# Performance work log

Hardware: AMD Instinct MI355X
Metric: run time of the kernel (lower is better)

Reference implementation:

```python
import jax, jax.numpy as jnp
import numpy as np
from jax import lax

# ---- config (matches DecodePredictions init kwargs) ----
MAX_PER_CLASS = 100
MAX_TOTAL = 100
IOU_THRESH = 0.5
SCORE_THRESH = 0.05
NUM_CLASSES = 80
K_CAND = 512  # per-class candidate pool kept before NMS (bounds the O(K^2) IoU work)
BOX_VARIANCE = np.array([0.1, 0.1, 0.2, 0.2], np.float32)


def generate_anchors(height, width):
    """RetinaNet anchors (keras.io AnchorBox): FPN levels 3-7, 3 ratios x 3 scales, [cx,cy,w,h] in pixels."""
    ratios = [0.5, 1.0, 2.0]
    scales = [2 ** 0.0, 2 ** (1.0 / 3.0), 2 ** (2.0 / 3.0)]
    all_anchors = []
    for level in range(3, 8):
        stride = 2 ** level
        area = float((2 ** (level + 2)) ** 2)  # 32^2 .. 512^2
        dims = []
        for r in ratios:
            ah = np.sqrt(area / r)
            aw = area / ah
            for s in scales:
                dims.append([s * aw, s * ah])
        dims = np.asarray(dims, np.float32)  # [9, 2] = (w, h)
        fh = int(np.ceil(height / stride))
        fw = int(np.ceil(width / stride))
        rx = (np.arange(fw, dtype=np.float32) + 0.5) * stride
        ry = (np.arange(fh, dtype=np.float32) + 0.5) * stride
        cx, cy = np.meshgrid(rx, ry)
        centers = np.stack([cx, cy], -1)[:, :, None, :].repeat(9, axis=2)  # [fh,fw,9,2]
        d = np.broadcast_to(dims, (fh, fw, 9, 2))
        all_anchors.append(np.concatenate([centers, d], -1).reshape(-1, 4).astype(np.float32))
    return jnp.asarray(np.concatenate(all_anchors, 0))  # [N, 4]


def _pairwise_iou(b):
    # Generic TF NMS IoU formula treating coords as [y1,x1,y2,x2] (module feeds cx,cy,w,h -- replicated faithfully).
    y1, x1, y2, x2 = b[:, 0], b[:, 1], b[:, 2], b[:, 3]
    area = jnp.maximum(y2 - y1, 0.0) * jnp.maximum(x2 - x1, 0.0)
    ih = jnp.maximum(jnp.minimum(y2[:, None], y2[None, :]) - jnp.maximum(y1[:, None], y1[None, :]), 0.0)
    iw = jnp.maximum(jnp.minimum(x2[:, None], x2[None, :]) - jnp.maximum(x1[:, None], x1[None, :]), 0.0)
    inter = ih * iw
    union = area[:, None] + area[None, :] - inter
    return jnp.where(union > 0.0, inter / union, 0.0)


def _nms_single_class(boxes, scores):  # boxes [N,4], scores [N]
    top_s, idx = lax.top_k(scores, K_CAND)          # sort-by-score candidate pool
    top_b = boxes[idx]                               # [K,4]
    keep0 = top_s > SCORE_THRESH                     # score_threshold filter
    iou = _pairwise_iou(top_b)                       # [K,K]
    rng = jnp.arange(K_CAND)

    def body(i, keep):
        sup = (iou[i] > IOU_THRESH) & (rng > i)      # boxes ranked below i suppressed by i
        return jnp.where(keep[i], keep & ~sup, keep)

    keep = lax.fori_loop(0, K_CAND, body, keep0)
    kept_s = jnp.where(keep, top_s, 0.0)
    sel_s, sel = lax.top_k(kept_s, MAX_PER_CLASS)    # max_output_size_per_class
    return top_b[sel], sel_s                         # [P,4], [P]


def _combine(cls_boxes, cls_scores):  # [C,P,4], [C,P] -> combined top MAX_TOTAL for one image
    C, P = cls_scores.shape
    flat_s = cls_scores.reshape(-1)
    flat_b = cls_boxes.reshape(-1, 4)
    flat_c = jnp.repeat(jnp.arange(C, dtype=jnp.float32), P)
    top_s, idx = lax.top_k(flat_s, MAX_TOTAL)
    valid = (top_s > 0.0)
    vf = valid.astype(flat_b.dtype)
    boxes = jnp.clip(flat_b[idx], 0.0, 1.0) * vf[:, None]  # clip_boxes=True, zero-pad invalid
    scores = top_s * vf
    classes = jnp.where(valid, flat_c[idx], 0.0)
    return boxes, scores, classes, valid.sum().astype(jnp.int32)


def _forward(inputs, predictions):
    H, W = inputs.shape[1], inputs.shape[2]
    anchors = generate_anchors(float(H), float(W))            # [N,4] cx,cy,w,h
    cls_scores = jax.nn.sigmoid(predictions[..., :-4])        # [B,N,C]
    box_pred = predictions[..., -4:] * jnp.asarray(BOX_VARIANCE)
    xy = box_pred[..., :2] * anchors[..., 2:] + anchors[..., :2]
    wh = jnp.exp(box_pred[..., 2:]) * anchors[..., 2:]
    boxes = jnp.concatenate([xy, wh], -1)                     # [B,N,4] decoded

    per_class = jax.vmap(jax.vmap(_nms_single_class, in_axes=(None, 1)), in_axes=(0, 0))
    cb, cs = per_class(boxes, cls_scores)                     # [B,C,P,4], [B,C,P]
    return jax.vmap(_combine)(cb, cs)                         # boxes, scores, classes, valid


def setup_inputs() -> dict:
    key = jax.random.key(0)
    k1, k2 = jax.random.split(key)
    inputs = jax.random.uniform(k1, (4, 640, 640, 3), jnp.float32)
    predictions = jax.random.normal(k2, (4, 76725, NUM_CLASSES + 4), jnp.float32)
    return {"inputs": inputs, "predictions": predictions}


def reference(inputs, predictions):
    return _forward(inputs, predictions)
```

## Files before the change

kernel.cpp:

```cpp
#include <hip/hip_runtime.h>
#include <cmath>

#define NA 76725
#define NCLS 80
#define NB 4
#define KC 512
#define MPC 100
#define MT 100
#define TT 64
#define LROW 85
#define NTILE 1199
#define NSLOTP 1199
#define NSLOTPAD 1216
#define PADN 76800
#define CAP 4096
#define SLOT 16
#define SPLIT 8
#define THRESH_LOGIT 2.0f

struct Dims { float d[5 * 9 * 2]; };


__device__ __forceinline__ unsigned keyof(float x) {
    unsigned u = __float_as_uint(x);
    return u ^ ((u & 0x80000000u) ? 0xFFFFFFFFu : 0x80000000u);
}
__device__ __forceinline__ float unkey(unsigned k) {
    unsigned u = (k & 0x80000000u) ? (k ^ 0x80000000u) : ~k;
    return __uint_as_float(u);
}
__device__ __forceinline__ float sigmoidf_dev(float x) {
    if (x >= 0.f) return 1.f / (1.f + expf(-x));
    float e = expf(x);
    return e / (1.f + e);
}
__device__ __forceinline__ unsigned long long compose(unsigned key, int a) {
    return ((unsigned long long)key << 32) | (unsigned long long)(0xFFFFFFFFu - (unsigned)a);
}

__device__ __forceinline__ float4 decode_box(float4 p, int a, const Dims& dims) {
    const int base[5] = {0, 57600, 72000, 75600, 76500};
    const int fw[5] = {80, 40, 20, 10, 5};
    const float strd[5] = {8.f, 16.f, 32.f, 64.f, 128.f};
    int l;
    if (a < 57600) l = 0;
    else if (a < 72000) l = 1;
    else if (a < 75600) l = 2;
    else if (a < 76500) l = 3;
    else l = 4;
    int i = a - base[l];
    int cell = i / 9, k = i - cell * 9;
    int x = cell % fw[l], y = cell / fw[l];
    float cx = ((float)x + 0.5f) * strd[l];
    float cy = ((float)y + 0.5f) * strd[l];
    float aw = dims.d[(l * 9 + k) * 2 + 0];
    float ah = dims.d[(l * 9 + k) * 2 + 1];
    float bx = __fmul_rn(p.x, 0.1f), by = __fmul_rn(p.y, 0.1f);
    float bw = __fmul_rn(p.z, 0.2f), bh = __fmul_rn(p.w, 0.2f);
    float4 o;
    o.x = __fadd_rn(__fmul_rn(bx, aw), cx);
    o.y = __fadd_rn(__fmul_rn(by, ah), cy);
    o.z = __fmul_rn(expf(bw), aw);
    o.w = __fmul_rn(expf(bh), ah);
    return o;
}


__global__ __launch_bounds__(256) void scan_kernel(const float* __restrict__ pred,
                                                   unsigned long long* __restrict__ candbuf,
                                                   int* __restrict__ counts2) {
    __shared__ float tile[TT * LROW];
    const int blk = blockIdx.x;
    const int b = blk / NTILE, tix = blk - b * NTILE;
    const int t0 = tix * TT;
    int nrow = NA - t0; if (nrow > TT) nrow = TT;

    const float4* src = reinterpret_cast<const float4*>(pred + ((size_t)b * NA + t0) * 84);
    const int nv = nrow * 21;
    for (int i = threadIdx.x; i < nv; i += 256) {
        float4 v = src[i];
        const int row = i / 21, fo = (i - row * 21) * 4;
        float* dst = &tile[row * LROW + fo];
        dst[0] = v.x; dst[1] = v.y; dst[2] = v.z; dst[3] = v.w;
    }
    __syncthreads();

    const int wv = threadIdx.x >> 6, lane = threadIdx.x & 63;
    const int c0 = wv * 20;
    const bool valid = lane < nrow;
    const int a = t0 + lane;
    const float* rowp = &tile[lane * LROW];

    int mycnt = 0;
    #pragma unroll
    for (int j = 0; j < 20; ++j) {
        const float x = valid ? rowp[c0 + j] : -1e30f;
        const bool hit = x > THRESH_LOGIT;
        const unsigned long long m = __ballot(hit);
        if (lane == j) mycnt = __popcll(m);
        if (hit) {
            const int rank = __popcll(m & ((1ull << lane) - 1ull));
            if (rank < SLOT) {
                const int col = b * NCLS + c0 + j;
                candbuf[((size_t)col * NSLOTP + tix) * SLOT + rank] = compose(keyof(x), a);
            }
        }
    }
    if (lane < 20)
        counts2[(size_t)(b * NCLS + c0 + lane) * NSLOTP + tix] = mycnt;
}


__device__ __forceinline__ void find_bin(int* hist, int bins, int remaining,
                                         int* sh3, int* wsum) {
    const int tid = threadIdx.x;
    const int lane = tid & 63, wv = tid >> 6;
    const int nit = (bins + 1023) >> 10;
    int lsum = 0;
    for (int q = 0; q < nit; ++q) {
        int rr = tid * nit + q;
        if (rr < bins) lsum += hist[bins - 1 - rr];
    }
    int acc = lsum;
    #pragma unroll
    for (int off = 1; off < 64; off <<= 1) {
        int x = __shfl_up(acc, off);
        if (lane >= off) acc += x;
    }
    if (lane == 63) wsum[wv] = acc;
    __syncthreads();
    int base = 0;
    for (int w = 0; w < wv; ++w) base += wsum[w];
    int run = base + acc - lsum;
    for (int q = 0; q < nit; ++q) {
        int rr = tid * nit + q;
        if (rr < bins) {
            int h = hist[bins - 1 - rr];
            if (run < remaining && remaining <= run + h) { sh3[0] = bins - 1 - rr; sh3[1] = run; sh3[2] = h; }
            run += h;
        }
    }
    __syncthreads();
}


__global__ __launch_bounds__(1024) void topk2_kernel(const float* __restrict__ pred,
                                                     const unsigned long long* __restrict__ candbuf,
                                                     const int* __restrict__ counts2,
                                                     int* __restrict__ top_idx,
                                                     float* __restrict__ top_score,
                                                     float4* __restrict__ sel_boxes, Dims dims) {
    const int col = blockIdx.x;
    const int b = col / NCLS, cc = col - b * NCLS;
    const int tid = threadIdx.x;
    const int lane = tid & 63, wv = tid >> 6;

    __shared__ unsigned long long cand[CAP];
    __shared__ int hist[256];
    __shared__ unsigned long long buf[KC];
    __shared__ int scnt[NSLOTPAD];
    __shared__ int spfx[NSLOTPAD];
    __shared__ int sh3[3];
    __shared__ int wsum[16];
    __shared__ int gcount, eqtaken, totsh, ovfsh;
    __shared__ int wcnt[16];
    int* hist4k = (int*)cand;

    for (int i = tid; i < NSLOTP; i += 1024)
        scnt[i] = counts2[(size_t)col * NSLOTP + i];
    if (tid < NSLOTPAD - NSLOTP) scnt[NSLOTP + tid] = 0;
    if (tid == 0) { totsh = 0; ovfsh = 0; }
    __syncthreads();

    const int e0 = 2 * tid, e1 = 2 * tid + 1;
    int c0s = 0, c1s = 0;
    if (e0 < NSLOTPAD) { c0s = scnt[e0]; c1s = scnt[e1]; }
    if (c0s > SLOT || c1s > SLOT) ovfsh = 1;
    const int pair = c0s + c1s;
    int acc = pair;
    #pragma unroll
    for (int off = 1; off < 64; off <<= 1) {
        int x = __shfl_up(acc, off);
        if (lane >= off) acc += x;
    }
    if (lane == 63) wsum[wv] = acc;
    __syncthreads();
    int base = 0;
    for (int w = 0; w < wv; ++w) base += wsum[w];
    if (e0 < NSLOTPAD) {
        const int excl = base + acc - pair;
        spfx[e0] = excl;
        spfx[e1] = excl + c0s;
    }
    if (tid == 1023) totsh = base + acc;
    __syncthreads();

    const int tot = totsh;
    const bool fastok = (!ovfsh) && tot >= KC && tot <= CAP;
    int nc = -1;

    if (fastok) {
        const unsigned long long* src = candbuf + (size_t)col * NSLOTP * SLOT;
        for (int i = tid; i < NSLOTP * SLOT; i += 1024) {
            const int e = i >> 4, q = i & (SLOT - 1);
            const unsigned long long v = src[i];
            if (q < scnt[e]) cand[spfx[e] + q] = v;
        }
        nc = tot;
        __syncthreads();
    } else {
        const float* colp = pred + (size_t)b * NA * 84 + cc;
        for (int i = tid; i < 4096; i += 1024) hist4k[i] = 0;
        __syncthreads();
        for (int a = tid; a < NA; a += 1024)
            atomicAdd(&hist4k[keyof(colp[(size_t)a * 84]) >> 20], 1);
        __syncthreads();
        find_bin(hist4k, 4096, KC, sh3, wsum);
        const int bsel = sh3[0], above = sh3[1], ceq1 = sh3[2];
        const int ncand = above + ceq1;

        if (ncand <= CAP) {
            const unsigned fk = ((unsigned)bsel) << 20;
            if (tid == 0) gcount = 0;
            __syncthreads();
            for (int a = tid; a < NA; a += 1024) {
                unsigned k = keyof(colp[(size_t)a * 84]);
                if (k >= fk) { int p = atomicAdd(&gcount, 1); cand[p] = compose(k, a); }
            }
            __syncthreads();
            nc = gcount;
        } else {
            unsigned prefix = ((unsigned)bsel) << 20;
            int remaining = KC - above;

            for (int i = tid; i < 4096; i += 1024) hist4k[i] = 0;
            __syncthreads();
            for (int a = tid; a < NA; a += 1024) {
                unsigned k = keyof(colp[(size_t)a * 84]);
                if ((k & 0xFFF00000u) == prefix) atomicAdd(&hist4k[(k >> 8) & 4095], 1);
            }
            __syncthreads();
            find_bin(hist4k, 4096, remaining, sh3, wsum);
            prefix |= ((unsigned)sh3[0]) << 8;
            remaining -= sh3[1];

            if (tid < 256) hist[tid] = 0;
            __syncthreads();
            for (int a = tid; a < NA; a += 1024) {
                unsigned k = keyof(colp[(size_t)a * 84]);
                if ((k & 0xFFFFFF00u) == prefix) atomicAdd(&hist[k & 255], 1);
            }
            __syncthreads();
            find_bin(hist, 256, remaining, sh3, wsum);
            prefix |= (unsigned)sh3[0];
            remaining -= sh3[1];

            const unsigned K = prefix;
            const int cgt = KC - remaining;
            const int need = remaining;
            if (tid == 0) { gcount = 0; eqtaken = 0; }
            __syncthreads();
            for (int bs = 0; bs < PADN; bs += 1024) {
                int a = bs + tid;
                unsigned key = (a < NA) ? keyof(colp[(size_t)a * 84]) : 0u;
                if (a < NA && key > K) {
                    int p = atomicAdd(&gcount, 1);
                    buf[p] = compose(key, a);
                }
                bool eq = (key == K) && (a < NA);
                unsigned long long m = __ballot(eq);
                if (lane == 0) wcnt[wv] = __popcll(m);
                __syncthreads();
                int off = eqtaken;
                for (int w = 0; w < wv; ++w) off += wcnt[w];
                int rank = off + __popcll(m & ((1ull << lane) - 1ull));
                if (eq && rank < need)
                    buf[cgt + rank] = compose(K, a);
                __syncthreads();
                if (tid == 0) {
                    int s = 0;
                    for (int w = 0; w < 16; ++w) s += wcnt[w];
                    eqtaken += s;
                }
                __syncthreads();
            }
            nc = -1;
        }
    }

    if (nc >= 0) {
        unsigned long long cpre = 0ull;
        int rem512 = KC;
        for (int pass = 0; pass < 8; ++pass) {
            const int shift = 56 - 8 * pass;
            const unsigned long long mdone = pass ? ((~0ull) << (shift + 8)) : 0ull;
            if (tid < 256) hist[tid] = 0;
            __syncthreads();
            for (int t = tid; t < nc; t += 1024) {
                unsigned long long k = cand[t];
                if ((k & mdone) == cpre) atomicAdd(&hist[(int)((k >> shift) & 255)], 1);
            }
            __syncthreads();
            find_bin(hist, 256, rem512, sh3, wsum);
            cpre |= ((unsigned long long)(unsigned)sh3[0]) << shift;
            rem512 -= sh3[1];
            __syncthreads();
        }
        if (tid == 0) gcount = 0;
        __syncthreads();
        for (int t = tid; t < nc; t += 1024) {
            unsigned long long k = cand[t];
            if (k >= cpre) { int p = atomicAdd(&gcount, 1); buf[p] = k; }
        }
        __syncthreads();
    }

    for (int k2 = 2; k2 <= KC; k2 <<= 1) {
        for (int j = k2 >> 1; j > 0; j >>= 1) {
            __syncthreads();
            if (tid < KC) {
                int i = tid, ixj = i ^ j;
                if (ixj > i) {
                    unsigned long long A = buf[i], B = buf[ixj];
                    bool up = (i & k2) == 0;
                    if (up ? (A < B) : (A > B)) { buf[i] = B; buf[ixj] = A; }
                }
            }
        }
    }
    __syncthreads();
    if (tid < KC) {
        unsigned long long v = buf[tid];
        unsigned key = (unsigned)(v >> 32);
        int a = (int)(0xFFFFFFFFu - (unsigned)(v & 0xFFFFFFFFu));
        top_idx[col * KC + tid] = a;
        top_score[col * KC + tid] = sigmoidf_dev(unkey(key));
        const float4 p4 = *reinterpret_cast<const float4*>(pred + ((size_t)b * NA + a) * 84 + 80);
        sel_boxes[(size_t)col * KC + tid] = decode_box(p4, a, dims);
    }
}


__global__ __launch_bounds__(512) void nms_build_kernel(const float4* __restrict__ sel_boxes,
                                                        unsigned long long* __restrict__ maskbuf) {
    const int blk = blockIdx.x;
    const int col = blk >> 3, part = blk & 7;
    const int tid = threadIdx.x, wave = tid >> 6, lane = tid & 63;
    __shared__ float y1[KC], x1[KC], y2[KC], x2[KC], ar[KC];

    for (int t = tid; t < KC; t += 512) {
        float4 bx = sel_boxes[(size_t)col * KC + t];
        y1[t] = bx.x; x1[t] = bx.y; y2[t] = bx.z; x2[t] = bx.w;
        ar[t] = __fmul_rn(fmaxf(__fsub_rn(bx.z, bx.x), 0.f),
                          fmaxf(__fsub_rn(bx.w, bx.y), 0.f));
    }
    __syncthreads();

    float jy1[8], jx1[8], jy2[8], jx2[8], jar[8];
    #pragma unroll
    for (int w = 0; w < 8; ++w) {
        int j = (w << 6) + lane;
        jy1[w] = y1[j]; jx1[w] = x1[j]; jy2[w] = y2[j]; jx2[w] = x2[j]; jar[w] = ar[j];
    }

    for (int k = 0; k < 8; ++k) {
        const int i = part + SPLIT * (wave + 8 * k);
        const float iy1 = y1[i], ix1 = x1[i], iy2 = y2[i], ix2 = x2[i], iar = ar[i];
        unsigned long long row[8];
        #pragma unroll
        for (int w = 0; w < 8; ++w) {
            unsigned long long m = 0ull;
            if (((w << 6) + 63) > i) {
                const int j = (w << 6) + lane;
                float ih = fmaxf(__fsub_rn(fminf(iy2, jy2[w]), fmaxf(iy1, jy1[w])), 0.f);
                float iw = fmaxf(__fsub_rn(fminf(ix2, jx2[w]), fmaxf(ix1, jx1[w])), 0.f);
                float inter = __fmul_rn(ih, iw);
                float uni = __fsub_rn(__fadd_rn(iar, jar[w]), inter);
                m = __ballot((uni > 0.f) && (inter > __fmul_rn(0.5f, uni)) && (j > i));
            }
            row[w] = m;
        }
        unsigned long long v = row[0];
        v = (lane == 1) ? row[1] : v;
        v = (lane == 2) ? row[2] : v;
        v = (lane == 3) ? row[3] : v;
        v = (lane == 4) ? row[4] : v;
        v = (lane == 5) ? row[5] : v;
        v = (lane == 6) ? row[6] : v;
        v = (lane == 7) ? row[7] : v;
        if (lane < 8) maskbuf[((size_t)col * KC + i) * 8 + lane] = v;
    }
}


__global__ __launch_bounds__(256) void nms_resolve_kernel(const float4* __restrict__ sel_boxes,
                                                          const float* __restrict__ top_score,
                                                          const unsigned long long* __restrict__ maskbuf,
                                                          float4* __restrict__ col_boxes,
                                                          float* __restrict__ col_scores) {
    const int col = blockIdx.x;
    const int tid = threadIdx.x, wv = tid >> 6, lane = tid & 63;
    __shared__ unsigned long long mask[KC * 8];
    __shared__ float y1[KC], x1[KC], y2[KC], x2[KC], sc[KC];
    __shared__ unsigned long long keep0w[8], keepw[8];
    __shared__ int wordpfx[9];
    __shared__ int sel[MPC];

    {
        const unsigned long long* src = maskbuf + (size_t)col * KC * 8;
        for (int m = tid; m < KC * 8; m += 256) mask[m] = src[m];
    }
    for (int t = tid; t < KC; t += 256) {
        float4 bx = sel_boxes[(size_t)col * KC + t];
        y1[t] = bx.x; x1[t] = bx.y; y2[t] = bx.z; x2[t] = bx.w;
        const float s = top_score[col * KC + t];
        sc[t] = s;
        const unsigned long long m = __ballot(s > 0.05f);
        if (lane == 0) keep0w[t >> 6] = m;
    }
    __syncthreads();

    if (wv == 0) {
        const int w8 = lane & 7;
        const unsigned long long kww = keep0w[w8];
        unsigned long long remw = 0ull;
        for (int ib = 0; ib < KC; ib += 8) {
            unsigned long long rows[8];
            #pragma unroll
            for (int u = 0; u < 8; ++u) rows[u] = mask[(ib + u) * 8 + w8];
            #pragma unroll
            for (int u = 0; u < 8; ++u) {
                const int i = ib + u, W = i >> 6, t = i & 63;
                const unsigned long long remW = __shfl(remw, W);
                const unsigned long long kwW = __shfl(kww, W);
                if (((kwW >> t) & 1ull) && !((remW >> t) & 1ull)) remw |= rows[u];
            }
        }
        if (lane < 8) keepw[w8] = kww & ~remw;
    }
    __syncthreads();
    if (tid == 0) {
        int s = 0;
        #pragma unroll
        for (int w = 0; w < 8; ++w) { wordpfx[w] = s; s += __popcll(keepw[w]); }
        wordpfx[8] = s;
    }
    __syncthreads();

    const int nkept = wordpfx[8];
    for (int t = tid; t < KC; t += 256) {
        const unsigned long long w = keepw[t >> 6];
        const int l = t & 63;
        const bool kp = (w >> l) & 1ull;
        const int kb = wordpfx[t >> 6] + __popcll(w & ((1ull << l) - 1ull));
        if (kp) {
            if (kb < MPC) sel[kb] = t;
        } else {
            const int nb = t - kb;
            if (nkept + nb < MPC) sel[nkept + nb] = t;
        }
    }
    __syncthreads();
    if (tid < MPC) {
        int t = sel[tid];
        bool kp = (keepw[t >> 6] >> (t & 63)) & 1ull;
        col_scores[col * MPC + tid] = kp ? sc[t] : 0.f;
        col_boxes[col * MPC + tid] = make_float4(y1[t], x1[t], y2[t], x2[t]);
    }
}


__global__ __launch_bounds__(256) void combine_kernel(const float4* __restrict__ col_boxes,
                                                      const float* __restrict__ col_scores,
                                                      float* __restrict__ out) {
    const int b = blockIdx.x, tid = threadIdx.x;
    const int wv = tid >> 6, lane = tid & 63;
    __shared__ int hist[256];
    __shared__ unsigned long long cand[128];
    __shared__ int sh3[3];
    __shared__ int gcnt, eqtaken;
    __shared__ int wcnt[4];
    __shared__ int wsc[4];

    unsigned sck[32];
    #pragma unroll
    for (int q = 0; q < 32; ++q) {
        const bool ok = (q < 31) || (tid < 64);
        sck[q] = ok ? __float_as_uint(col_scores[b * NCLS * MPC + (q << 8) + tid]) : 0u;
    }

    unsigned prefix = 0;
    int remaining = MT, ceq = 0;
    #pragma unroll 1
    for (int pass = 0; pass < 4; ++pass) {
        const int shift = 24 - 8 * pass;
        const unsigned mdone = pass ? (0xFFFFFFFFu << (shift + 8)) : 0u;
        hist[tid] = 0;
        __syncthreads();
        #pragma unroll
        for (int q = 0; q < 32; ++q) {
            const bool ok = (q < 31) || (tid < 64);
            if (ok && (sck[q] & mdone) == prefix)
                atomicAdd(&hist[(sck[q] >> shift) & 255], 1);
        }
        __syncthreads();
        int lsum = hist[255 - tid];
        int acc2 = lsum;
        #pragma unroll
        for (int off = 1; off < 64; off <<= 1) {
            int x = __shfl_up(acc2, off);
            if (lane >= off) acc2 += x;
        }
        if (lane == 63) wsc[wv] = acc2;
        __syncthreads();
        int base2 = 0;
        for (int w = 0; w < wv; ++w) base2 += wsc[w];
        int run = base2 + acc2 - lsum;
        if (run < remaining && remaining <= run + lsum) { sh3[0] = 255 - tid; sh3[1] = run; sh3[2] = lsum; }
        __syncthreads();
        prefix |= ((unsigned)sh3[0]) << shift;
        remaining -= sh3[1];
        ceq = sh3[2];
        __syncthreads();
    }
    const unsigned S = prefix;
    const int cgt = MT - remaining;

    if (tid == 0) { gcnt = 0; eqtaken = 0; }
    if (tid < 128) cand[tid] = 0ull;
    __syncthreads();
    #pragma unroll
    for (int q = 0; q < 32; ++q) {
        const bool ok = (q < 31) || (tid < 64);
        if (ok && sck[q] > S) {
            int p = atomicAdd(&gcnt, 1);
            int t = (q << 8) + tid;
            cand[p] = ((unsigned long long)sck[q] << 32) |
                      (unsigned long long)(0xFFFFFFFFu - (unsigned)t);
        }
    }
    __syncthreads();

    if (ceq == remaining) {
        #pragma unroll
        for (int q = 0; q < 32; ++q) {
            const bool ok = (q < 31) || (tid < 64);
            if (ok && sck[q] == S) {
                int p = atomicAdd(&eqtaken, 1);
                int t = (q << 8) + tid;
                cand[cgt + p] = ((unsigned long long)S << 32) |
                                (unsigned long long)(0xFFFFFFFFu - (unsigned)t);
            }
        }
        __syncthreads();
    } else {
        #pragma unroll 1
        for (int q = 0; q < 32; ++q) {
            const bool ok = (q < 31) || (tid < 64);
            const bool eq = ok && (sck[q] == S);
            unsigned long long m = __ballot(eq);
            if (lane == 0) wcnt[wv] = __popcll(m);
            __syncthreads();
            int off = eqtaken;
            for (int w = 0; w < wv; ++w) off += wcnt[w];
            int rank = off + __popcll(m & ((1ull << lane) - 1ull));
            if (eq && rank < remaining) {
                int t = (q << 8) + tid;
                cand[cgt + rank] = ((unsigned long long)S << 32) |
                                   (unsigned long long)(0xFFFFFFFFu - (unsigned)t);
            }
            __syncthreads();
            if (tid == 0) eqtaken += wcnt[0] + wcnt[1] + wcnt[2] + wcnt[3];
            __syncthreads();
        }
    }

    for (int k2 = 2; k2 <= 128; k2 <<= 1) {
        for (int j = k2 >> 1; j > 0; j >>= 1) {
            __syncthreads();
            if (tid < 128) {
                int i = tid, ixj = i ^ j;
                if (ixj > i) {
                    unsigned long long A = cand[i], B = cand[ixj];
                    bool up = (i & k2) == 0;
                    if (up ? (A < B) : (A > B)) { cand[i] = B; cand[ixj] = A; }
                }
            }
        }
    }
    __syncthreads();
    if (tid == 0) gcnt = 0;
    __syncthreads();
    if (tid < MT) {
        unsigned long long v = cand[tid];
        float s = __uint_as_float((unsigned)(v >> 32));
        int f = (int)(0xFFFFFFFFu - (unsigned)(v & 0xFFFFFFFFu));
        bool valid = (s > 0.f);
        int cl = 0, p = 0;
        float4 bx = make_float4(0.f, 0.f, 0.f, 0.f);
        if (valid) {
            cl = f / MPC;
            p = f - cl * MPC;
            float4 raw = col_boxes[((size_t)b * NCLS + cl) * MPC + p];
            bx.x = fminf(fmaxf(raw.x, 0.f), 1.f);
            bx.y = fminf(fmaxf(raw.y, 0.f), 1.f);
            bx.z = fminf(fmaxf(raw.z, 0.f), 1.f);
            bx.w = fminf(fmaxf(raw.w, 0.f), 1.f);
            atomicAdd(&gcnt, 1);
        }
        int o = b * MT + tid;
        out[o * 4 + 0] = bx.x;
        out[o * 4 + 1] = bx.y;
        out[o * 4 + 2] = bx.z;
        out[o * 4 + 3] = bx.w;
        out[NB * MT * 4 + o] = valid ? s : 0.f;
        out[NB * MT * 5 + o] = valid ? (float)cl : 0.f;
    }
    __syncthreads();
    if (tid == 0) out[NB * MT * 6 + b] = (float)gcnt;
}


extern "C" void kernel_launch(void* const* d_in, const int* in_sizes, int n_in,
                              void* d_out, int out_size, void* d_ws, size_t ws_size,
                              hipStream_t stream) {
    const float* pred = (const float*)d_in[1];
    float* out = (float*)d_out;
    char* ws = (char*)d_ws;

    Dims dims;
    const double ratios[3] = {0.5, 1.0, 2.0};
    for (int l = 0; l < 5; ++l) {
        double side = (double)(1 << (l + 5));
        double area = side * side;
        for (int ri = 0; ri < 3; ++ri) {
            double ah = sqrt(area / ratios[ri]);
            double aw = area / ah;
            for (int si = 0; si < 3; ++si) {
                double s = pow(2.0, (double)si / 3.0);
                dims.d[(l * 9 + ri * 3 + si) * 2 + 0] = (float)(s * aw);
                dims.d[(l * 9 + ri * 3 + si) * 2 + 1] = (float)(s * ah);
            }
        }
    }

    const size_t SZ_CAND  = (size_t)NB * NCLS * NSLOTP * SLOT * 8;
    const size_t SZ_CNT   = (size_t)NB * NCLS * NSLOTP * 4;
    const size_t SZ_TOPI  = (size_t)NB * NCLS * KC * 4;
    const size_t SZ_SEL   = (size_t)NB * NCLS * KC * 16;
    const size_t SZ_CB    = (size_t)NB * NCLS * MPC * 16;

    unsigned long long* candbuf    = (unsigned long long*)(ws);
    int*                counts2    = (int*)(ws + SZ_CAND);
    int*                top_idx    = (int*)(ws + SZ_CAND + SZ_CNT);
    float*              top_score  = (float*)(ws + SZ_CAND + SZ_CNT + SZ_TOPI);
    float4*             sel_boxes  = (float4*)(ws + SZ_CAND + SZ_CNT + 2 * SZ_TOPI);
    float4*             col_boxes  = (float4*)(ws + SZ_CAND + SZ_CNT + 2 * SZ_TOPI + SZ_SEL);
    float*              col_scores = (float*)(ws + SZ_CAND + SZ_CNT + 2 * SZ_TOPI + SZ_SEL + SZ_CB);
    unsigned long long* maskbuf    = (unsigned long long*)(ws);

    scan_kernel<<<NB * NTILE, 256, 0, stream>>>(pred, candbuf, counts2);
    topk2_kernel<<<NB * NCLS, 1024, 0, stream>>>(pred, candbuf, counts2, top_idx, top_score, sel_boxes, dims);
    nms_build_kernel<<<NB * NCLS * SPLIT, 512, 0, stream>>>(sel_boxes, maskbuf);
    nms_resolve_kernel<<<NB * NCLS, 256, 0, stream>>>(sel_boxes, top_score, maskbuf, col_boxes, col_scores);
    combine_kernel<<<NB, 256, 0, stream>>>(col_boxes, col_scores, out);
}
```

Before: 338.6 us.

## Scan tiles of 128 anchors with shared-memory atomics and widen combine to 1024 threads

The scan kernel now tests logits straight from the loaded float4 registers instead of staging a 64-row tile in shared memory. Per-class slot positions come from shared-memory atomic counters, and each tile covers 128 anchors, so there are half as many slot groups per class. The top-k kernel scans 600 slot counts with one thread each, has less candidate buffer to compact, and no longer writes the unused top_idx array. The combine kernel uses 1024 threads with 8 scores per thread instead of 256 threads with 32. In exchange, candidate order inside a slot becomes nondeterministic, and larger tiles make it more likely a class overflows its 16 slots and drops to the slow fallback path.

```diff
diff --git a/kernel.cpp b/kernel.cpp
--- a/kernel.cpp
+++ b/kernel.cpp
@@ -7,11 +7,9 @@
 #define KC 512
 #define MPC 100
 #define MT 100
-#define TT 64
-#define LROW 85
-#define NTILE 1199
-#define NSLOTP 1199
-#define NSLOTPAD 1216
+#define TT 128
+#define NTILE 600
+#define NSLOTP 600
 #define PADN 76800
 #define CAP 4096
 #define SLOT 16
@@ -69,45 +67,37 @@
 __global__ __launch_bounds__(256) void scan_kernel(const float* __restrict__ pred,
                                                    unsigned long long* __restrict__ candbuf,
                                                    int* __restrict__ counts2) {
-    __shared__ float tile[TT * LROW];
+    __shared__ int cnt[NCLS];
     const int blk = blockIdx.x;
     const int b = blk / NTILE, tix = blk - b * NTILE;
     const int t0 = tix * TT;
     int nrow = NA - t0; if (nrow > TT) nrow = TT;
 
+    if (threadIdx.x < NCLS) cnt[threadIdx.x] = 0;
+    __syncthreads();
+
     const float4* src = reinterpret_cast<const float4*>(pred + ((size_t)b * NA + t0) * 84);
     const int nv = nrow * 21;
+    unsigned long long* slotbase = candbuf + (size_t)(b * NCLS) * NSLOTP * SLOT + (size_t)tix * SLOT;
     for (int i = threadIdx.x; i < nv; i += 256) {
-        float4 v = src[i];
-        const int row = i / 21, fo = (i - row * 21) * 4;
-        float* dst = &tile[row * LROW + fo];
-        dst[0] = v.x; dst[1] = v.y; dst[2] = v.z; dst[3] = v.w;
-    }
-    __syncthreads();
-
-    const int wv = threadIdx.x >> 6, lane = threadIdx.x & 63;
-    const int c0 = wv * 20;
-    const bool valid = lane < nrow;
-    const int a = t0 + lane;
-    const float* rowp = &tile[lane * LROW];
-
-    int mycnt = 0;
-    #pragma unroll
-    for (int j = 0; j < 20; ++j) {
-        const float x = valid ? rowp[c0 + j] : -1e30f;
-        const bool hit = x > THRESH_LOGIT;
-        const unsigned long long m = __ballot(hit);
-        if (lane == j) mycnt = __popcll(m);
-        if (hit) {
-            const int rank = __popcll(m & ((1ull << lane) - 1ull));
-            if (rank < SLOT) {
-                const int col = b * NCLS + c0 + j;
-                candbuf[((size_t)col * NSLOTP + tix) * SLOT + rank] = compose(keyof(x), a);
-            }
-        }
-    }
-    if (lane < 20)
-        counts2[(size_t)(b * NCLS + c0 + lane) * NSLOTP + tix] = mycnt;
+        const float4 v = src[i];
+        const int row = i / 21, chunk = i - row * 21;
+        if (chunk == 20) continue;
+        const int a = t0 + row, cbase = chunk * 4;
+        const float vals[4] = {v.x, v.y, v.z, v.w};
+        #pragma unroll
+        for (int q = 0; q < 4; ++q) {
+            if (vals[q] > THRESH_LOGIT) {
+                const int c = cbase + q;
+                const int p = atomicAdd(&cnt[c], 1);
+                if (p < SLOT)
+                    slotbase[(size_t)c * NSLOTP * SLOT + p] = compose(keyof(vals[q]), a);
+            }
+        }
+    }
+    __syncthreads();
+    if (threadIdx.x < NCLS)
+        counts2[(size_t)(b * NCLS + threadIdx.x) * NSLOTP + tix] = cnt[threadIdx.x];
 }
 
 
@@ -147,7 +137,6 @@
 __global__ __launch_bounds__(1024) void topk2_kernel(const float* __restrict__ pred,
                                                      const unsigned long long* __restrict__ candbuf,
                                                      const int* __restrict__ counts2,
-                                                     int* __restrict__ top_idx,
                                                      float* __restrict__ top_score,
                                                      float4* __restrict__ sel_boxes, Dims dims) {
     const int col = blockIdx.x;
@@ -158,26 +147,21 @@
     __shared__ unsigned long long cand[CAP];
     __shared__ int hist[256];
     __shared__ unsigned long long buf[KC];
-    __shared__ int scnt[NSLOTPAD];
-    __shared__ int spfx[NSLOTPAD];
+    __shared__ int scnt[NSLOTP];
+    __shared__ int spfx[NSLOTP];
     __shared__ int sh3[3];
     __shared__ int wsum[16];
     __shared__ int gcount, eqtaken, totsh, ovfsh;
     __shared__ int wcnt[16];
     int* hist4k = (int*)cand;
 
-    for (int i = tid; i < NSLOTP; i += 1024)
-        scnt[i] = counts2[(size_t)col * NSLOTP + i];
-    if (tid < NSLOTPAD - NSLOTP) scnt[NSLOTP + tid] = 0;
     if (tid == 0) { totsh = 0; ovfsh = 0; }
-    __syncthreads();
-
-    const int e0 = 2 * tid, e1 = 2 * tid + 1;
-    int c0s = 0, c1s = 0;
-    if (e0 < NSLOTPAD) { c0s = scnt[e0]; c1s = scnt[e1]; }
-    if (c0s > SLOT || c1s > SLOT) ovfsh = 1;
-    const int pair = c0s + c1s;
-    int acc = pair;
+    if (tid < NSLOTP) scnt[tid] = counts2[(size_t)col * NSLOTP + tid];
+    __syncthreads();
+
+    int lsum = (tid < NSLOTP) ? scnt[tid] : 0;
+    if (lsum > SLOT) ovfsh = 1;
+    int acc = lsum;
     #pragma unroll
     for (int off = 1; off < 64; off <<= 1) {
         int x = __shfl_up(acc, off);
@@ -187,11 +171,7 @@
     __syncthreads();
     int base = 0;
     for (int w = 0; w < wv; ++w) base += wsum[w];
-    if (e0 < NSLOTPAD) {
-        const int excl = base + acc - pair;
-        spfx[e0] = excl;
-        spfx[e1] = excl + c0s;
-    }
+    if (tid < NSLOTP) spfx[tid] = base + acc - lsum;
     if (tid == 1023) totsh = base + acc;
     __syncthreads();
 
@@ -333,7 +313,6 @@
         unsigned long long v = buf[tid];
         unsigned key = (unsigned)(v >> 32);
         int a = (int)(0xFFFFFFFFu - (unsigned)(v & 0xFFFFFFFFu));
-        top_idx[col * KC + tid] = a;
         top_score[col * KC + tid] = sigmoidf_dev(unkey(key));
         const float4 p4 = *reinterpret_cast<const float4*>(pred + ((size_t)b * NA + a) * 84 + 80);
         sel_boxes[(size_t)col * KC + tid] = decode_box(p4, a, dims);
@@ -470,23 +449,24 @@
 }
 
 
-__global__ __launch_bounds__(256) void combine_kernel(const float4* __restrict__ col_boxes,
-                                                      const float* __restrict__ col_scores,
-                                                      float* __restrict__ out) {
+__global__ __launch_bounds__(1024) void combine_kernel(const float4* __restrict__ col_boxes,
+                                                       const float* __restrict__ col_scores,
+                                                       float* __restrict__ out) {
     const int b = blockIdx.x, tid = threadIdx.x;
     const int wv = tid >> 6, lane = tid & 63;
     __shared__ int hist[256];
     __shared__ unsigned long long cand[128];
     __shared__ int sh3[3];
     __shared__ int gcnt, eqtaken;
-    __shared__ int wcnt[4];
-    __shared__ int wsc[4];
-
-    unsigned sck[32];
+    __shared__ int wcnt[16];
+    __shared__ int wsc[16];
+
+    const int NTOT = NCLS * MPC;
+    unsigned sck[8];
     #pragma unroll
-    for (int q = 0; q < 32; ++q) {
-        const bool ok = (q < 31) || (tid < 64);
-        sck[q] = ok ? __float_as_uint(col_scores[b * NCLS * MPC + (q << 8) + tid]) : 0u;
+    for (int q = 0; q < 8; ++q) {
+        const int t = (q << 10) + tid;
+        sck[q] = (t < NTOT) ? __float_as_uint(col_scores[b * NTOT + t]) : 0u;
     }
 
     unsigned prefix = 0;
@@ -495,16 +475,16 @@
     for (int pass = 0; pass < 4; ++pass) {
         const int shift = 24 - 8 * pass;
         const unsigned mdone = pass ? (0xFFFFFFFFu << (shift + 8)) : 0u;
-        hist[tid] = 0;
+        if (tid < 256) hist[tid] = 0;
         __syncthreads();
         #pragma unroll
-        for (int q = 0; q < 32; ++q) {
-            const bool ok = (q < 31) || (tid < 64);
-            if (ok && (sck[q] & mdone) == prefix)
+        for (int q = 0; q < 8; ++q) {
+            const int t = (q << 10) + tid;
+            if (t < NTOT && (sck[q] & mdone) == prefix)
                 atomicAdd(&hist[(sck[q] >> shift) & 255], 1);
         }
         __syncthreads();
-        int lsum = hist[255 - tid];
+        int lsum = (tid < 256) ? hist[255 - tid] : 0;
         int acc2 = lsum;
         #pragma unroll
         for (int off = 1; off < 64; off <<= 1) {
@@ -516,7 +496,7 @@
         int base2 = 0;
         for (int w = 0; w < wv; ++w) base2 += wsc[w];
         int run = base2 + acc2 - lsum;
-        if (run < remaining && remaining <= run + lsum) { sh3[0] = 255 - tid; sh3[1] = run; sh3[2] = lsum; }
+        if (tid < 256 && run < remaining && remaining <= run + lsum) { sh3[0] = 255 - tid; sh3[1] = run; sh3[2] = lsum; }
         __syncthreads();
         prefix |= ((unsigned)sh3[0]) << shift;
         remaining -= sh3[1];
@@ -530,11 +510,10 @@
     if (tid < 128) cand[tid] = 0ull;
     __syncthreads();
     #pragma unroll
-    for (int q = 0; q < 32; ++q) {
-        const bool ok = (q < 31) || (tid < 64);
-        if (ok && sck[q] > S) {
+    for (int q = 0; q < 8; ++q) {
+        const int t = (q << 10) + tid;
+        if (t < NTOT && sck[q] > S) {
             int p = atomicAdd(&gcnt, 1);
-            int t = (q << 8) + tid;
             cand[p] = ((unsigned long long)sck[q] << 32) |
                       (unsigned long long)(0xFFFFFFFFu - (unsigned)t);
         }
@@ -543,11 +522,10 @@
 
     if (ceq == remaining) {
         #pragma unroll
-        for (int q = 0; q < 32; ++q) {
-            const bool ok = (q < 31) || (tid < 64);
-            if (ok && sck[q] == S) {
+        for (int q = 0; q < 8; ++q) {
+            const int t = (q << 10) + tid;
+            if (t < NTOT && sck[q] == S) {
                 int p = atomicAdd(&eqtaken, 1);
-                int t = (q << 8) + tid;
                 cand[cgt + p] = ((unsigned long long)S << 32) |
                                 (unsigned long long)(0xFFFFFFFFu - (unsigned)t);
             }
@@ -555,22 +533,24 @@
         __syncthreads();
     } else {
         #pragma unroll 1
-        for (int q = 0; q < 32; ++q) {
-            const bool ok = (q < 31) || (tid < 64);
-            const bool eq = ok && (sck[q] == S);
+        for (int q = 0; q < 8; ++q) {
+            const int t = (q << 10) + tid;
+            const bool eq = (t < NTOT) && (sck[q] == S);
             unsigned long long m = __ballot(eq);
             if (lane == 0) wcnt[wv] = __popcll(m);
             __syncthreads();
             int off = eqtaken;
             for (int w = 0; w < wv; ++w) off += wcnt[w];
             int rank = off + __popcll(m & ((1ull << lane) - 1ull));
-            if (eq && rank < remaining) {
-                int t = (q << 8) + tid;
+            if (eq && rank < remaining)
                 cand[cgt + rank] = ((unsigned long long)S << 32) |
                                    (unsigned long long)(0xFFFFFFFFu - (unsigned)t);
-            }
-            __syncthreads();
-            if (tid == 0) eqtaken += wcnt[0] + wcnt[1] + wcnt[2] + wcnt[3];
+            __syncthreads();
+            if (tid == 0) {
+                int s = 0;
+                for (int w = 0; w < 16; ++w) s += wcnt[w];
+                eqtaken += s;
+            }
             __syncthreads();
         }
     }
@@ -644,24 +624,23 @@
         }
     }
 
-    const size_t SZ_CAND  = (size_t)NB * NCLS * NSLOTP * SLOT * 8;
-    const size_t SZ_CNT   = (size_t)NB * NCLS * NSLOTP * 4;
-    const size_t SZ_TOPI  = (size_t)NB * NCLS * KC * 4;
-    const size_t SZ_SEL   = (size_t)NB * NCLS * KC * 16;
-    const size_t SZ_CB    = (size_t)NB * NCLS * MPC * 16;
+    const size_t SZ_CAND = (size_t)NB * NCLS * NSLOTP * SLOT * 8;
+    const size_t SZ_CNT  = (size_t)NB * NCLS * NSLOTP * 4;
+    const size_t SZ_SC   = (size_t)NB * NCLS * KC * 4;
+    const size_t SZ_SEL  = (size_t)NB * NCLS * KC * 16;
+    const size_t SZ_CB   = (size_t)NB * NCLS * MPC * 16;
 
     unsigned long long* candbuf    = (unsigned long long*)(ws);
     int*                counts2    = (int*)(ws + SZ_CAND);
-    int*                top_idx    = (int*)(ws + SZ_CAND + SZ_CNT);
-    float*              top_score  = (float*)(ws + SZ_CAND + SZ_CNT + SZ_TOPI);
-    float4*             sel_boxes  = (float4*)(ws + SZ_CAND + SZ_CNT + 2 * SZ_TOPI);
-    float4*             col_boxes  = (float4*)(ws + SZ_CAND + SZ_CNT + 2 * SZ_TOPI + SZ_SEL);
-    float*              col_scores = (float*)(ws + SZ_CAND + SZ_CNT + 2 * SZ_TOPI + SZ_SEL + SZ_CB);
+    float*              top_score  = (float*)(ws + SZ_CAND + SZ_CNT);
+    float4*             sel_boxes  = (float4*)(ws + SZ_CAND + SZ_CNT + SZ_SC);
+    float4*             col_boxes  = (float4*)(ws + SZ_CAND + SZ_CNT + SZ_SC + SZ_SEL);
+    float*              col_scores = (float*)(ws + SZ_CAND + SZ_CNT + SZ_SC + SZ_SEL + SZ_CB);
     unsigned long long* maskbuf    = (unsigned long long*)(ws);
 
     scan_kernel<<<NB * NTILE, 256, 0, stream>>>(pred, candbuf, counts2);
-    topk2_kernel<<<NB * NCLS, 1024, 0, stream>>>(pred, candbuf, counts2, top_idx, top_score, sel_boxes, dims);
+    topk2_kernel<<<NB * NCLS, 1024, 0, stream>>>(pred, candbuf, counts2, top_score, sel_boxes, dims);
     nms_build_kernel<<<NB * NCLS * SPLIT, 512, 0, stream>>>(sel_boxes, maskbuf);
     nms_resolve_kernel<<<NB * NCLS, 256, 0, stream>>>(sel_boxes, top_score, maskbuf, col_boxes, col_scores);
-    combine_kernel<<<NB, 256, 0, stream>>>(col_boxes, col_scores, out);
-}
+    combine_kernel<<<NB, 1024, 0, stream>>>(col_boxes, col_scores, out);
+}
```

After: 321.8 us. 1.05x faster.
